# Kernel tuning notes

Measured on AMD Instinct MI355X. Metric: run time of the kernel, lower is better.

The kernel has to match this reference:

```python
import jax, jax.numpy as jnp
import numpy as np

B, C, Q, D = 64, 1024, 256, 128
NEG = -1e30  # VERY_NEGATIVE_NUMBER


def setup_inputs() -> dict:
    key = jax.random.key(0)
    k1, k2, k3, k4, k5, k6 = jax.random.split(key, 6)
    return {
        "x_cont": jax.random.normal(k1, (B, C, D), dtype=jnp.float32),
        "x_ques": jax.random.normal(k2, (B, Q, D), dtype=jnp.float32),
        "c_mask": jnp.ones((B, C), dtype=jnp.float32),
        "q_mask": jnp.ones((B, Q), dtype=jnp.float32),
        "W0": jax.random.uniform(k3, (D, 1), jnp.float32, -0.1, 0.1),
        "W1": jax.random.uniform(k4, (D, 1), jnp.float32, -0.1, 0.1),
        "W2": jax.random.uniform(k5, (1, 1, D), jnp.float32, -0.1, 0.1),
        "bias": jnp.zeros((1,), dtype=jnp.float32),
    }


def reference(x_cont, x_ques, c_mask, q_mask, W0, W1, W2, bias):
    # Trilinear similarity S[b,c,q] = x_cont.W0 + x_ques.W1 + (x_cont*W2).x_ques^T + bias
    s0 = x_cont @ W0                                   # [B,C,1]
    s1 = jnp.swapaxes(x_ques @ W1, 1, 2)               # [B,1,Q]
    s2 = jnp.einsum('bcd,bqd->bcq', x_cont * W2, x_ques)  # [B,C,Q]
    S = s0 + s1 + s2 + bias                            # [B,C,Q]

    qm = q_mask[:, None, :]                            # [B,1,Q]
    cm = c_mask[:, :, None]                            # [B,C,1]
    S_ = jax.nn.softmax(S + NEG * (1.0 - qm), axis=-1)           # row softmax [B,C,Q]
    S_T = jnp.swapaxes(jax.nn.softmax(S + NEG * (1.0 - cm), axis=1), 1, 2)  # [B,Q,C]

    c2q = S_ @ x_ques                                  # [B,C,D]
    q2c = (S_ @ S_T) @ x_cont                          # [B,C,D]
    return jnp.concatenate([x_cont, c2q, x_cont * c2q, x_cont * q2c], axis=-1)
```

## Files before the change

kernel.cpp:

```cpp
#include <hip/hip_runtime.h>
#include <math.h>

#define BB 64
#define CC 1024
#define QQ 256
#define DD 128
#define NEGV (-1.0e30f)

typedef short bf8 __attribute__((ext_vector_type(8)));
typedef short bf4 __attribute__((ext_vector_type(4)));
typedef float f4v __attribute__((ext_vector_type(4)));

__device__ __forceinline__ short f2bf(float f) {
    unsigned u = __builtin_bit_cast(unsigned, f);
    u += 0x7FFFu + ((u >> 16) & 1u);
    return (short)(u >> 16);
}
__device__ __forceinline__ float bf2f(short s) {
    unsigned u = ((unsigned)(unsigned short)s) << 16;
    return __builtin_bit_cast(float, u);
}

template <int MULW2>
__global__ __launch_bounds__(256, 2) void k0_fused(const float* __restrict__ src,
                                                   const float* __restrict__ W,
                                                   const float* __restrict__ W2,
                                                   const float* __restrict__ mask,
                                                   float* __restrict__ sm,
                                                   short* __restrict__ rm,
                                                   short* __restrict__ tr, int R) {
    __shared__ float tile[64][132];
    int tiles = R >> 6;
    int b = blockIdx.x / tiles, tl = blockIdx.x - b * tiles;
    int r0 = tl * 64;
    int t = threadIdx.x;
    int c4 = t & 31, rr = t >> 5;
    float4 wv = ((const float4*)W)[c4];
    float4 w2v{};
    if constexpr (MULW2) w2v = ((const float4*)W2)[c4];
    const float* sb = src + ((size_t)b * R + r0) * DD;
    #pragma unroll
    for (int p = 0; p < 8; ++p) {
        int row = rr + p * 8;
        float4 g = *(const float4*)&sb[(size_t)row * DD + c4 * 4];
        bf4 o;
        if constexpr (MULW2) {
            o[0] = f2bf(g.x * w2v.x); o[1] = f2bf(g.y * w2v.y);
            o[2] = f2bf(g.z * w2v.z); o[3] = f2bf(g.w * w2v.w);
        } else {
            o[0] = f2bf(g.x); o[1] = f2bf(g.y);
            o[2] = f2bf(g.z); o[3] = f2bf(g.w);
        }
        *(bf4*)&rm[((size_t)(b * R + r0 + row)) * DD + c4 * 4] = o;
        float part = g.x * wv.x + g.y * wv.y + g.z * wv.z + g.w * wv.w;
        #pragma unroll
        for (int off = 1; off < 32; off <<= 1) part += __shfl_xor(part, off, 64);
        if ((t & 31) == 0)
            sm[(size_t)b * R + r0 + row] =
                part + NEGV * (1.0f - mask[(size_t)b * R + r0 + row]);
        *(float4*)&tile[row][c4 * 4] = g;
    }
    __syncthreads();
    int d = t >> 1, rh = (t & 1) * 32;
    #pragma unroll
    for (int k = 0; k < 8; ++k) {
        bf4 o;
        #pragma unroll
        for (int i = 0; i < 4; ++i) o[i] = f2bf(tile[rh + k * 4 + i][d]);
        *(bf4*)&tr[((size_t)(b * DD + d)) * R + r0 + rh + k * 4] = o;
    }
}

#define SCP 1032
#define S2P 264
#define XTP 72

__global__ __launch_bounds__(256, 3) void k1_colsm(
        const short* __restrict__ xc_bf, const short* __restrict__ xcT_bf,
        const short* __restrict__ xqw_bf, const float* __restrict__ s0m,
        short* __restrict__ AT) {
    __shared__ __align__(16) short sc[16][SCP];
    __shared__ __align__(16) short xct[DD][XTP];
    __shared__ float invl[16];

    int bid = blockIdx.x;
    int qt = (bid >> 3) & 15;
    int b = ((bid >> 7) << 3) | (bid & 7);
    int q0 = qt * 16;
    int t = threadIdx.x, w = t >> 6, l = t & 63;
    int quad = l >> 4, l16 = l & 15;

    bf8 bq[4];
    {
        const short* qp = &xqw_bf[(size_t)(b * QQ + q0 + l16) * DD + quad * 8];
        #pragma unroll
        for (int ks = 0; ks < 4; ++ks) bq[ks] = *(const bf8*)&qp[ks * 32];
    }

    const short* abase = &xc_bf[(size_t)(b * CC + w * 16 + l16) * DD + quad * 8];
    const float* s0base = &s0m[b * CC + w * 16 + quad * 4];
    bf8 cur[4];
    #pragma unroll
    for (int ks = 0; ks < 4; ++ks) cur[ks] = *(const bf8*)&abase[ks * 32];
    #pragma unroll
    for (int ct = 0; ct < 16; ++ct) {
        bf8 nxt[4];
        if (ct < 15) {
            const short* ar = abase + (size_t)(ct + 1) * 64 * DD;
            #pragma unroll
            for (int ks = 0; ks < 4; ++ks) nxt[ks] = *(const bf8*)&ar[ks * 32];
        }
        f4v acc = {0.f, 0.f, 0.f, 0.f};
        #pragma unroll
        for (int ks = 0; ks < 4; ++ks)
            acc = __builtin_amdgcn_mfma_f32_16x16x32_bf16(cur[ks], bq[ks], acc, 0, 0, 0);
        f4v s0v = *(const f4v*)&s0base[ct * 64];
        bf4 ov;
        #pragma unroll
        for (int r = 0; r < 4; ++r) ov[r] = f2bf(acc[r] + s0v[r]);
        *(bf4*)&sc[l16][ct * 64 + w * 16 + quad * 4] = ov;
        #pragma unroll
        for (int ks = 0; ks < 4; ++ks) cur[ks] = nxt[ks];
    }

    int c8 = t & 7, dr = t >> 3;
    const short* tbase = &xcT_bf[(size_t)(b * DD + dr) * CC + c8 * 8];
    bf8 g[4];
    #pragma unroll
    for (int p = 0; p < 4; ++p)
        g[p] = *(const bf8*)&tbase[(size_t)(p * 32) * CC];

    __syncthreads();

    {
        int q = t >> 4, k = t & 15;
        float m = -3.0e38f;
        #pragma unroll 8
        for (int i = 0; i < 64; ++i) m = fmaxf(m, bf2f(sc[q][k + 16 * i]));
        #pragma unroll
        for (int off = 1; off < 16; off <<= 1) m = fmaxf(m, __shfl_xor(m, off, 64));
        float sum = 0.f;
        #pragma unroll 8
        for (int i = 0; i < 64; ++i) {
            int idx = k + 16 * i;
            float e = __expf(bf2f(sc[q][idx]) - m);
            sc[q][idx] = f2bf(e);
            sum += e;
        }
        #pragma unroll
        for (int off = 1; off < 16; off <<= 1) sum += __shfl_xor(sum, off, 64);
        if (k == 0) invl[q] = 1.0f / sum;
    }
    __syncthreads();

    f4v acc0 = {0.f, 0.f, 0.f, 0.f}, acc1 = {0.f, 0.f, 0.f, 0.f};
    for (int ct = 0; ct < 16; ++ct) {
        #pragma unroll
        for (int p = 0; p < 4; ++p)
            *(bf8*)&xct[dr + p * 32][c8 * 8] = g[p];
        if (ct < 15) {
            #pragma unroll
            for (int p = 0; p < 4; ++p)
                g[p] = *(const bf8*)&tbase[(size_t)(p * 32) * CC + (ct + 1) * 64];
        }
        __syncthreads();
        #pragma unroll
        for (int ks = 0; ks < 2; ++ks) {
            bf8 a = *(const bf8*)&sc[l16][ct * 64 + ks * 32 + quad * 8];
            bf8 b0 = *(const bf8*)&xct[w * 32 + l16][ks * 32 + quad * 8];
            acc0 = __builtin_amdgcn_mfma_f32_16x16x32_bf16(a, b0, acc0, 0, 0, 0);
            bf8 b1 = *(const bf8*)&xct[w * 32 + 16 + l16][ks * 32 + quad * 8];
            acc1 = __builtin_amdgcn_mfma_f32_16x16x32_bf16(a, b1, acc1, 0, 0, 0);
        }
        __syncthreads();
    }
    {
        bf4 o0, o1;
        #pragma unroll
        for (int r = 0; r < 4; ++r) {
            float il = invl[quad * 4 + r];
            o0[r] = f2bf(acc0[r] * il);
            o1[r] = f2bf(acc1[r] * il);
        }
        int d0 = w * 32 + l16;
        *(bf4*)&AT[(size_t)(b * DD + d0) * QQ + q0 + quad * 4] = o0;
        *(bf4*)&AT[(size_t)(b * DD + d0 + 16) * QQ + q0 + quad * 4] = o1;
    }
}

__global__ __launch_bounds__(256, 4) void k2_rowsm(
        const float* __restrict__ xc, const short* __restrict__ xc_bf,
        const short* __restrict__ xqw_bf, const short* __restrict__ xqT_bf,
        const short* __restrict__ AT, const float* __restrict__ s1m,
        float* __restrict__ out) {
    __shared__ __align__(16) short sc2[32][S2P];
    __shared__ __align__(16) short tT[DD][XTP];
    __shared__ float invl2[32];

    int bid = blockIdx.x;
    int cb = (bid >> 3) & 31;
    int b = ((bid >> 8) << 3) | (bid & 7);
    int c0g = cb * 32;
    int t = threadIdx.x, w = t >> 6, l = t & 63;
    int quad = l >> 4, l16 = l & 15;

    bf8 bc0[4], bc1[4];
    {
        const short* p0 = &xc_bf[(size_t)(b * CC + c0g + l16) * DD + quad * 8];
        const short* p1 = p0 + 16 * DD;
        #pragma unroll
        for (int ks = 0; ks < 4; ++ks) {
            bc0[ks] = *(const bf8*)&p0[ks * 32];
            bc1[ks] = *(const bf8*)&p1[ks * 32];
        }
    }

    const short* abase = &xqw_bf[(size_t)(b * QQ + w * 16 + l16) * DD + quad * 8];
    const float* s1base = &s1m[b * QQ + w * 16 + quad * 4];
    bf8 cur[4];
    #pragma unroll
    for (int ks = 0; ks < 4; ++ks) cur[ks] = *(const bf8*)&abase[ks * 32];
    #pragma unroll
    for (int qt = 0; qt < 4; ++qt) {
        bf8 nxt[4];
        if (qt < 3) {
            const short* ar = abase + (size_t)(qt + 1) * 64 * DD;
            #pragma unroll
            for (int ks = 0; ks < 4; ++ks) nxt[ks] = *(const bf8*)&ar[ks * 32];
        }
        f4v acc0 = {0.f, 0.f, 0.f, 0.f}, acc1 = {0.f, 0.f, 0.f, 0.f};
        #pragma unroll
        for (int ks = 0; ks < 4; ++ks) {
            acc0 = __builtin_amdgcn_mfma_f32_16x16x32_bf16(cur[ks], bc0[ks], acc0, 0, 0, 0);
            acc1 = __builtin_amdgcn_mfma_f32_16x16x32_bf16(cur[ks], bc1[ks], acc1, 0, 0, 0);
        }
        int qbase = qt * 64 + w * 16 + quad * 4;
        f4v sv = *(const f4v*)&s1base[qt * 64];
        bf4 o0, o1;
        #pragma unroll
        for (int r = 0; r < 4; ++r) {
            o0[r] = f2bf(acc0[r] + sv[r]);
            o1[r] = f2bf(acc1[r] + sv[r]);
        }
        *(bf4*)&sc2[l16][qbase] = o0;
        *(bf4*)&sc2[16 + l16][qbase] = o1;
        #pragma unroll
        for (int ks = 0; ks < 4; ++ks) cur[ks] = nxt[ks];
    }

    int q8 = t & 7, dr = t >> 3;
    const short* qtb = &xqT_bf[(size_t)(b * DD + dr) * QQ + q8 * 8];
    const short* atb = &AT[(size_t)(b * DD + dr) * QQ + q8 * 8];
    bf8 g[4];
    #pragma unroll
    for (int p = 0; p < 4; ++p)
        g[p] = *(const bf8*)&qtb[(size_t)(p * 32) * QQ];

    __syncthreads();

    {
        int c = t >> 3, k = t & 7;
        float m = -3.0e38f;
        #pragma unroll 8
        for (int i = 0; i < 32; ++i) m = fmaxf(m, bf2f(sc2[c][k + 8 * i]));
        #pragma unroll
        for (int off = 1; off < 8; off <<= 1) m = fmaxf(m, __shfl_xor(m, off, 64));
        float sum = 0.f;
        #pragma unroll 8
        for (int i = 0; i < 32; ++i) {
            int idx = k + 8 * i;
            float e = __expf(bf2f(sc2[c][idx]) - m);
            sc2[c][idx] = f2bf(e);
            sum += e;
        }
        #pragma unroll
        for (int off = 1; off < 8; off <<= 1) sum += __shfl_xor(sum, off, 64);
        if (k == 0) invl2[c] = 1.0f / sum;
    }
    __syncthreads();

    int cb16 = (w & 1) * 16, dh = (w >> 1) * 64;
    f4v ac[4], aq[4];
    f4v zz = {0.f, 0.f, 0.f, 0.f};
    #pragma unroll
    for (int n = 0; n < 4; ++n) { ac[n] = zz; aq[n] = zz; }
    #pragma unroll
    for (int tl = 0; tl < 8; ++tl) {
        #pragma unroll
        for (int p = 0; p < 4; ++p)
            *(bf8*)&tT[dr + p * 32][q8 * 8] = g[p];
        if (tl < 7) {
            const short* s = (tl + 1 < 4) ? qtb : atb;
            int qq = ((tl + 1) & 3) * 64;
            #pragma unroll
            for (int p = 0; p < 4; ++p)
                g[p] = *(const bf8*)&s[(size_t)(p * 32) * QQ + qq];
        }
        __syncthreads();
        int qt = tl & 3;
        #pragma unroll
        for (int ks = 0; ks < 2; ++ks) {
            bf8 a = *(const bf8*)&sc2[cb16 + l16][qt * 64 + ks * 32 + quad * 8];
            #pragma unroll
            for (int n = 0; n < 4; ++n) {
                bf8 bb = *(const bf8*)&tT[dh + n * 16 + l16][ks * 32 + quad * 8];
                if (tl < 4) ac[n] = __builtin_amdgcn_mfma_f32_16x16x32_bf16(a, bb, ac[n], 0, 0, 0);
                else        aq[n] = __builtin_amdgcn_mfma_f32_16x16x32_bf16(a, bb, aq[n], 0, 0, 0);
            }
        }
        __syncthreads();
    }

    #pragma unroll
    for (int r = 0; r < 4; ++r) {
        int c = c0g + cb16 + quad * 4 + r;
        float il = invl2[cb16 + quad * 4 + r];
        const float* xrow = xc + (size_t)(b * CC + c) * DD;
        float* orow = out + (size_t)(b * CC + c) * (4 * DD);
        #pragma unroll
        for (int n = 0; n < 4; ++n) {
            int d = dh + n * 16 + l16;
            float xv = xrow[d];
            float c2v = ac[n][r] * il;
            float q2v = aq[n][r] * il;
            orow[d] = xv;
            orow[DD + d] = c2v;
            orow[2 * DD + d] = xv * c2v;
            orow[3 * DD + d] = xv * q2v;
        }
    }
}

extern "C" void kernel_launch(void* const* d_in, const int* in_sizes, int n_in,
                              void* d_out, int out_size, void* d_ws, size_t ws_size,
                              hipStream_t stream) {
    const float* x_cont = (const float*)d_in[0];
    const float* x_ques = (const float*)d_in[1];
    const float* c_mask = (const float*)d_in[2];
    const float* q_mask = (const float*)d_in[3];
    const float* W0     = (const float*)d_in[4];
    const float* W1     = (const float*)d_in[5];
    const float* W2     = (const float*)d_in[6];
    float* out = (float*)d_out;

    char* ws = (char*)d_ws;
    float* s0m    = (float*)ws;  ws += (size_t)BB * CC * 4;
    float* s1m    = (float*)ws;  ws += (size_t)BB * QQ * 4;
    short* xc_bf  = (short*)ws;  ws += (size_t)BB * CC * DD * 2;
    short* xqw_bf = (short*)ws;  ws += (size_t)BB * QQ * DD * 2;
    short* xcT_bf = (short*)ws;  ws += (size_t)BB * CC * DD * 2;
    short* xqT_bf = (short*)ws;  ws += (size_t)BB * QQ * DD * 2;
    short* AT     = (short*)ws;

    k0_fused<0><<<BB * (CC / 64), 256, 0, stream>>>(x_cont, W0, nullptr, c_mask,
                                                    s0m, xc_bf, xcT_bf, CC);
    k0_fused<1><<<BB * (QQ / 64), 256, 0, stream>>>(x_ques, W1, W2, q_mask,
                                                    s1m, xqw_bf, xqT_bf, QQ);
    k1_colsm<<<BB * 16, 256, 0, stream>>>(xc_bf, xcT_bf, xqw_bf, s0m, AT);
    k2_rowsm<<<BB * 32, 256, 0, stream>>>(x_cont, xc_bf, xqw_bf, xqT_bf, AT, s1m, out);
}
```

Baseline: 277.2 us.

## Load MFMA B operands directly from global with register prefetch, merge prep kernels

```diff
diff --git a/kernel.cpp b/kernel.cpp
--- a/kernel.cpp
+++ b/kernel.cpp
@@ -21,36 +21,40 @@
     return __builtin_bit_cast(float, u);
 }
 
-template <int MULW2>
-__global__ __launch_bounds__(256, 2) void k0_fused(const float* __restrict__ src,
-                                                   const float* __restrict__ W,
-                                                   const float* __restrict__ W2,
-                                                   const float* __restrict__ mask,
-                                                   float* __restrict__ sm,
-                                                   short* __restrict__ rm,
-                                                   short* __restrict__ tr, int R) {
-    __shared__ float tile[64][132];
-    int tiles = R >> 6;
-    int b = blockIdx.x / tiles, tl = blockIdx.x - b * tiles;
+__global__ __launch_bounds__(256, 2) void k0_all(
+        const float* __restrict__ xc, const float* __restrict__ xq,
+        const float* __restrict__ W0, const float* __restrict__ W1,
+        const float* __restrict__ W2,
+        const float* __restrict__ c_mask, const float* __restrict__ q_mask,
+        float* __restrict__ s0m, float* __restrict__ s1m,
+        short* __restrict__ xc_bf, short* __restrict__ xqw_bf,
+        short* __restrict__ xcT_bf, short* __restrict__ xqT_bf) {
+    __shared__ float tile[64][129];
+    int bid = blockIdx.x;
+    const float *src, *W, *mask;
+    float* sm; short *rm, *tr;
+    int b, tl, R; bool use2;
+    if (bid < 1024) {
+        b = ((bid >> 7) << 3) | (bid & 7); tl = (bid >> 3) & 15; R = CC;
+        src = xc; W = W0; mask = c_mask; sm = s0m; rm = xc_bf; tr = xcT_bf; use2 = false;
+    } else {
+        int q = bid - 1024;
+        b = ((q >> 5) << 3) | (q & 7); tl = (q >> 3) & 3; R = QQ;
+        src = xq; W = W1; mask = q_mask; sm = s1m; rm = xqw_bf; tr = xqT_bf; use2 = true;
+    }
     int r0 = tl * 64;
     int t = threadIdx.x;
     int c4 = t & 31, rr = t >> 5;
     float4 wv = ((const float4*)W)[c4];
-    float4 w2v{};
-    if constexpr (MULW2) w2v = ((const float4*)W2)[c4];
+    float4 sc4 = use2 ? ((const float4*)W2)[c4] : make_float4(1.f, 1.f, 1.f, 1.f);
     const float* sb = src + ((size_t)b * R + r0) * DD;
     #pragma unroll
     for (int p = 0; p < 8; ++p) {
         int row = rr + p * 8;
         float4 g = *(const float4*)&sb[(size_t)row * DD + c4 * 4];
         bf4 o;
-        if constexpr (MULW2) {
-            o[0] = f2bf(g.x * w2v.x); o[1] = f2bf(g.y * w2v.y);
-            o[2] = f2bf(g.z * w2v.z); o[3] = f2bf(g.w * w2v.w);
-        } else {
-            o[0] = f2bf(g.x); o[1] = f2bf(g.y);
-            o[2] = f2bf(g.z); o[3] = f2bf(g.w);
-        }
+        o[0] = f2bf(g.x * sc4.x); o[1] = f2bf(g.y * sc4.y);
+        o[2] = f2bf(g.z * sc4.z); o[3] = f2bf(g.w * sc4.w);
         *(bf4*)&rm[((size_t)(b * R + r0 + row)) * DD + c4 * 4] = o;
         float part = g.x * wv.x + g.y * wv.y + g.z * wv.z + g.w * wv.w;
         #pragma unroll
@@ -58,29 +62,29 @@
         if ((t & 31) == 0)
             sm[(size_t)b * R + r0 + row] =
                 part + NEGV * (1.0f - mask[(size_t)b * R + r0 + row]);
-        *(float4*)&tile[row][c4 * 4] = g;
-    }
-    __syncthreads();
-    int d = t >> 1, rh = (t & 1) * 32;
-    #pragma unroll
-    for (int k = 0; k < 8; ++k) {
-        bf4 o;
-        #pragma unroll
-        for (int i = 0; i < 4; ++i) o[i] = f2bf(tile[rh + k * 4 + i][d]);
-        *(bf4*)&tr[((size_t)(b * DD + d)) * R + r0 + rh + k * 4] = o;
+        tile[row][c4 * 4 + 0] = g.x; tile[row][c4 * 4 + 1] = g.y;
+        tile[row][c4 * 4 + 2] = g.z; tile[row][c4 * 4 + 3] = g.w;
+    }
+    __syncthreads();
+    int rj = (t & 7) * 8;
+    #pragma unroll
+    for (int pp = 0; pp < 4; ++pp) {
+        int d = pp * 32 + (t >> 3);
+        bf8 o;
+        #pragma unroll
+        for (int j = 0; j < 8; ++j) o[j] = f2bf(tile[rj + j][d]);
+        *(bf8*)&tr[((size_t)(b * DD + d)) * R + r0 + rj] = o;
     }
 }
 
 #define SCP 1032
 #define S2P 264
-#define XTP 72
 
 __global__ __launch_bounds__(256, 3) void k1_colsm(
         const short* __restrict__ xc_bf, const short* __restrict__ xcT_bf,
         const short* __restrict__ xqw_bf, const float* __restrict__ s0m,
         short* __restrict__ AT) {
     __shared__ __align__(16) short sc[16][SCP];
-    __shared__ __align__(16) short xct[DD][XTP];
     __shared__ float invl[16];
 
     int bid = blockIdx.x;
@@ -119,18 +123,24 @@
         #pragma unroll
         for (int r = 0; r < 4; ++r) ov[r] = f2bf(acc[r] + s0v[r]);
         *(bf4*)&sc[l16][ct * 64 + w * 16 + quad * 4] = ov;
-        #pragma unroll
-        for (int ks = 0; ks < 4; ++ks) cur[ks] = nxt[ks];
-    }
-
-    int c8 = t & 7, dr = t >> 3;
-    const short* tbase = &xcT_bf[(size_t)(b * DD + dr) * CC + c8 * 8];
-    bf8 g[4];
-    #pragma unroll
-    for (int p = 0; p < 4; ++p)
-        g[p] = *(const bf8*)&tbase[(size_t)(p * 32) * CC];
-
-    __syncthreads();
+        if (ct < 15) {
+            #pragma unroll
+            for (int ks = 0; ks < 4; ++ks) cur[ks] = nxt[ks];
+        }
+    }
+    __syncthreads();
+
+    const short* b0base = &xcT_bf[(size_t)(b * DD + w * 32 + l16) * CC + quad * 8];
+    const short* b1base = b0base + (size_t)16 * CC;
+    bf8 pb[3][4];
+    #pragma unroll
+    for (int i = 0; i < 3; ++i) {
+        #pragma unroll
+        for (int ks = 0; ks < 2; ++ks) {
+            pb[i][ks]     = *(const bf8*)&b0base[i * 64 + ks * 32];
+            pb[i][2 + ks] = *(const bf8*)&b1base[i * 64 + ks * 32];
+        }
+    }
 
     {
         int q = t >> 4, k = t & 15;
@@ -154,25 +164,26 @@
     __syncthreads();
 
     f4v acc0 = {0.f, 0.f, 0.f, 0.f}, acc1 = {0.f, 0.f, 0.f, 0.f};
+    #pragma unroll
     for (int ct = 0; ct < 16; ++ct) {
-        #pragma unroll
-        for (int p = 0; p < 4; ++p)
-            *(bf8*)&xct[dr + p * 32][c8 * 8] = g[p];
-        if (ct < 15) {
-            #pragma unroll
-            for (int p = 0; p < 4; ++p)
-                g[p] = *(const bf8*)&tbase[(size_t)(p * 32) * CC + (ct + 1) * 64];
-        }
-        __syncthreads();
-        #pragma unroll
-        for (int ks = 0; ks < 2; ++ks) {
-            bf8 a = *(const bf8*)&sc[l16][ct * 64 + ks * 32 + quad * 8];
-            bf8 b0 = *(const bf8*)&xct[w * 32 + l16][ks * 32 + quad * 8];
-            acc0 = __builtin_amdgcn_mfma_f32_16x16x32_bf16(a, b0, acc0, 0, 0, 0);
-            bf8 b1 = *(const bf8*)&xct[w * 32 + 16 + l16][ks * 32 + quad * 8];
-            acc1 = __builtin_amdgcn_mfma_f32_16x16x32_bf16(a, b1, acc1, 0, 0, 0);
-        }
-        __syncthreads();
+        bf8 c00 = pb[0][0], c01 = pb[0][1], c10 = pb[0][2], c11 = pb[0][3];
+        #pragma unroll
+        for (int i = 0; i < 2; ++i)
+            #pragma unroll
+            for (int j = 0; j < 4; ++j) pb[i][j] = pb[i + 1][j];
+        if (ct + 3 < 16) {
+            #pragma unroll
+            for (int ks = 0; ks < 2; ++ks) {
+                pb[2][ks]     = *(const bf8*)&b0base[(ct + 3) * 64 + ks * 32];
+                pb[2][2 + ks] = *(const bf8*)&b1base[(ct + 3) * 64 + ks * 32];
+            }
+        }
+        bf8 a0 = *(const bf8*)&sc[l16][ct * 64 + quad * 8];
+        bf8 a1 = *(const bf8*)&sc[l16][ct * 64 + 32 + quad * 8];
+        acc0 = __builtin_amdgcn_mfma_f32_16x16x32_bf16(a0, c00, acc0, 0, 0, 0);
+        acc0 = __builtin_amdgcn_mfma_f32_16x16x32_bf16(a1, c01, acc0, 0, 0, 0);
+        acc1 = __builtin_amdgcn_mfma_f32_16x16x32_bf16(a0, c10, acc1, 0, 0, 0);
+        acc1 = __builtin_amdgcn_mfma_f32_16x16x32_bf16(a1, c11, acc1, 0, 0, 0);
     }
     {
         bf4 o0, o1;
@@ -188,13 +199,12 @@
     }
 }
 
-__global__ __launch_bounds__(256, 4) void k2_rowsm(
+__global__ __launch_bounds__(256, 3) void k2_rowsm(
         const float* __restrict__ xc, const short* __restrict__ xc_bf,
         const short* __restrict__ xqw_bf, const short* __restrict__ xqT_bf,
         const short* __restrict__ AT, const float* __restrict__ s1m,
         float* __restrict__ out) {
     __shared__ __align__(16) short sc2[32][S2P];
-    __shared__ __align__(16) short tT[DD][XTP];
     __shared__ float invl2[32];
 
     int bid = blockIdx.x;
@@ -244,19 +254,24 @@
         }
         *(bf4*)&sc2[l16][qbase] = o0;
         *(bf4*)&sc2[16 + l16][qbase] = o1;
-        #pragma unroll
-        for (int ks = 0; ks < 4; ++ks) cur[ks] = nxt[ks];
-    }
-
-    int q8 = t & 7, dr = t >> 3;
-    const short* qtb = &xqT_bf[(size_t)(b * DD + dr) * QQ + q8 * 8];
-    const short* atb = &AT[(size_t)(b * DD + dr) * QQ + q8 * 8];
-    bf8 g[4];
-    #pragma unroll
-    for (int p = 0; p < 4; ++p)
-        g[p] = *(const bf8*)&qtb[(size_t)(p * 32) * QQ];
-
-    __syncthreads();
+        if (qt < 3) {
+            #pragma unroll
+            for (int ks = 0; ks < 4; ++ks) cur[ks] = nxt[ks];
+        }
+    }
+    __syncthreads();
+
+    const short* gq = &xqT_bf[(size_t)(b * DD + w * 32 + l16) * QQ + quad * 8];
+    const short* ga = &AT[(size_t)(b * DD + w * 32 + l16) * QQ + quad * 8];
+    bf8 pb[3][4];
+    #pragma unroll
+    for (int i = 0; i < 3; ++i) {
+        #pragma unroll
+        for (int ks = 0; ks < 2; ++ks) {
+            pb[i][ks]     = *(const bf8*)&gq[i * 64 + ks * 32];
+            pb[i][2 + ks] = *(const bf8*)&gq[(size_t)16 * QQ + i * 64 + ks * 32];
+        }
+    }
 
     {
         int c = t >> 3, k = t & 7;
@@ -279,56 +294,76 @@
     }
     __syncthreads();
 
-    int cb16 = (w & 1) * 16, dh = (w >> 1) * 64;
-    f4v ac[4], aq[4];
+    f4v ac[2][2], aq[2][2];
     f4v zz = {0.f, 0.f, 0.f, 0.f};
     #pragma unroll
-    for (int n = 0; n < 4; ++n) { ac[n] = zz; aq[n] = zz; }
+    for (int i = 0; i < 2; ++i)
+        #pragma unroll
+        for (int j = 0; j < 2; ++j) { ac[i][j] = zz; aq[i][j] = zz; }
     #pragma unroll
     for (int tl = 0; tl < 8; ++tl) {
-        #pragma unroll
-        for (int p = 0; p < 4; ++p)
-            *(bf8*)&tT[dr + p * 32][q8 * 8] = g[p];
-        if (tl < 7) {
-            const short* s = (tl + 1 < 4) ? qtb : atb;
-            int qq = ((tl + 1) & 3) * 64;
-            #pragma unroll
-            for (int p = 0; p < 4; ++p)
-                g[p] = *(const bf8*)&s[(size_t)(p * 32) * QQ + qq];
-        }
-        __syncthreads();
-        int qt = tl & 3;
-        #pragma unroll
-        for (int ks = 0; ks < 2; ++ks) {
-            bf8 a = *(const bf8*)&sc2[cb16 + l16][qt * 64 + ks * 32 + quad * 8];
-            #pragma unroll
-            for (int n = 0; n < 4; ++n) {
-                bf8 bb = *(const bf8*)&tT[dh + n * 16 + l16][ks * 32 + quad * 8];
-                if (tl < 4) ac[n] = __builtin_amdgcn_mfma_f32_16x16x32_bf16(a, bb, ac[n], 0, 0, 0);
-                else        aq[n] = __builtin_amdgcn_mfma_f32_16x16x32_bf16(a, bb, aq[n], 0, 0, 0);
+        bf8 c00 = pb[0][0], c01 = pb[0][1], c10 = pb[0][2], c11 = pb[0][3];
+        #pragma unroll
+        for (int i = 0; i < 2; ++i)
+            #pragma unroll
+            for (int j = 0; j < 4; ++j) pb[i][j] = pb[i + 1][j];
+        if (tl + 3 < 8) {
+            int nt = tl + 3;
+            const short* gs = (nt < 4) ? (gq + (size_t)(nt) * 64)
+                                       : (ga + (size_t)(nt - 4) * 64);
+            #pragma unroll
+            for (int ks = 0; ks < 2; ++ks) {
+                pb[2][ks]     = *(const bf8*)&gs[ks * 32];
+                pb[2][2 + ks] = *(const bf8*)&gs[(size_t)16 * QQ + ks * 32];
             }
         }
-        __syncthreads();
-    }
-
-    #pragma unroll
-    for (int r = 0; r < 4; ++r) {
-        int c = c0g + cb16 + quad * 4 + r;
-        float il = invl2[cb16 + quad * 4 + r];
-        const float* xrow = xc + (size_t)(b * CC + c) * DD;
-        float* orow = out + (size_t)(b * CC + c) * (4 * DD);
-        #pragma unroll
-        for (int n = 0; n < 4; ++n) {
-            int d = dh + n * 16 + l16;
-            float xv = xrow[d];
-            float c2v = ac[n][r] * il;
-            float q2v = aq[n][r] * il;
-            orow[d] = xv;
-            orow[DD + d] = c2v;
-            orow[2 * DD + d] = xv * c2v;
-            orow[3 * DD + d] = xv * q2v;
-        }
-    }
+        int qoff = (tl & 3) * 64;
+        bf8 a00 = *(const bf8*)&sc2[l16][qoff + quad * 8];
+        bf8 a01 = *(const bf8*)&sc2[l16][qoff + 32 + quad * 8];
+        bf8 a10 = *(const bf8*)&sc2[16 + l16][qoff + quad * 8];
+        bf8 a11 = *(const bf8*)&sc2[16 + l16][qoff + 32 + quad * 8];
+        if (tl < 4) {
+            ac[0][0] = __builtin_amdgcn_mfma_f32_16x16x32_bf16(a00, c00, ac[0][0], 0, 0, 0);
+            ac[0][0] = __builtin_amdgcn_mfma_f32_16x16x32_bf16(a01, c01, ac[0][0], 0, 0, 0);
+            ac[0][1] = __builtin_amdgcn_mfma_f32_16x16x32_bf16(a00, c10, ac[0][1], 0, 0, 0);
+            ac[0][1] = __builtin_amdgcn_mfma_f32_16x16x32_bf16(a01, c11, ac[0][1], 0, 0, 0);
+            ac[1][0] = __builtin_amdgcn_mfma_f32_16x16x32_bf16(a10, c00, ac[1][0], 0, 0, 0);
+            ac[1][0] = __builtin_amdgcn_mfma_f32_16x16x32_bf16(a11, c01, ac[1][0], 0, 0, 0);
+            ac[1][1] = __builtin_amdgcn_mfma_f32_16x16x32_bf16(a10, c10, ac[1][1], 0, 0, 0);
+            ac[1][1] = __builtin_amdgcn_mfma_f32_16x16x32_bf16(a11, c11, ac[1][1], 0, 0, 0);
+        } else {
+            aq[0][0] = __builtin_amdgcn_mfma_f32_16x16x32_bf16(a00, c00, aq[0][0], 0, 0, 0);
+            aq[0][0] = __builtin_amdgcn_mfma_f32_16x16x32_bf16(a01, c01, aq[0][0], 0, 0, 0);
+            aq[0][1] = __builtin_amdgcn_mfma_f32_16x16x32_bf16(a00, c10, aq[0][1], 0, 0, 0);
+            aq[0][1] = __builtin_amdgcn_mfma_f32_16x16x32_bf16(a01, c11, aq[0][1], 0, 0, 0);
+            aq[1][0] = __builtin_amdgcn_mfma_f32_16x16x32_bf16(a10, c00, aq[1][0], 0, 0, 0);
+            aq[1][0] = __builtin_amdgcn_mfma_f32_16x16x32_bf16(a11, c01, aq[1][0], 0, 0, 0);
+            aq[1][1] = __builtin_amdgcn_mfma_f32_16x16x32_bf16(a10, c10, aq[1][1], 0, 0, 0);
+            aq[1][1] = __builtin_amdgcn_mfma_f32_16x16x32_bf16(a11, c11, aq[1][1], 0, 0, 0);
+        }
+    }
+
+    #pragma unroll
+    for (int cf = 0; cf < 2; ++cf)
+        #pragma unroll
+        for (int r = 0; r < 4; ++r) {
+            int cl = cf * 16 + quad * 4 + r;
+            int c = c0g + cl;
+            float il = invl2[cl];
+            const float* xrow = xc + (size_t)(b * CC + c) * DD;
+            float* orow = out + (size_t)(b * CC + c) * (4 * DD);
+            #pragma unroll
+            for (int df = 0; df < 2; ++df) {
+                int d = w * 32 + df * 16 + l16;
+                float xv = xrow[d];
+                float c2v = ac[cf][df][r] * il;
+                float q2v = aq[cf][df][r] * il;
+                orow[d] = xv;
+                orow[DD + d] = c2v;
+                orow[2 * DD + d] = xv * c2v;
+                orow[3 * DD + d] = xv * q2v;
+            }
+        }
 }
 
 extern "C" void kernel_launch(void* const* d_in, const int* in_sizes, int n_in,
@@ -352,10 +387,9 @@
     short* xqT_bf = (short*)ws;  ws += (size_t)BB * QQ * DD * 2;
     short* AT     = (short*)ws;
 
-    k0_fused<0><<<BB * (CC / 64), 256, 0, stream>>>(x_cont, W0, nullptr, c_mask,
-                                                    s0m, xc_bf, xcT_bf, CC);
-    k0_fused<1><<<BB * (QQ / 64), 256, 0, stream>>>(x_ques, W1, W2, q_mask,
-                                                    s1m, xqw_bf, xqT_bf, QQ);
+    k0_all<<<BB * 16 + BB * 4, 256, 0, stream>>>(x_cont, x_ques, W0, W1, W2,
+                                                 c_mask, q_mask, s0m, s1m,
+                                                 xc_bf, xqw_bf, xcT_bf, xqT_bf);
     k1_colsm<<<BB * 16, 256, 0, stream>>>(xc_bf, xcT_bf, xqw_bf, s0m, AT);
     k2_rowsm<<<BB * 32, 256, 0, stream>>>(x_cont, xc_bf, xqw_bf, xqT_bf, AT, s1m, out);
 }
```

New measurement: 296.4 us. 1.07x slower.
